# Optimization experiments

Hardware: AMD Instinct MI355X
Metric: run time of the kernel (lower is better)

Reference implementation:

```python
import jax, jax.numpy as jnp
import numpy as np

NUM_HEADS = 12

def _elu1(x):
    return jax.nn.elu(x) + 1.0

def setup_inputs() -> dict:
    key = jax.random.key(0)
    ks = jax.random.split(key, 7)
    B, Nq, Nk, D = 8, 4096, 1024, 768
    s = 0.02
    return {
        "x_query": jax.random.normal(ks[0], (B, Nq, D), dtype=jnp.float32),
        "x_key_value": jax.random.normal(ks[1], (B, Nk, D), dtype=jnp.float32),
        "Wq": jax.random.normal(ks[2], (D, D), dtype=jnp.float32) * s,
        "Wk": jax.random.normal(ks[3], (D, D), dtype=jnp.float32) * s,
        "Wv": jax.random.normal(ks[4], (D, D), dtype=jnp.float32) * s,
        "Wo": jax.random.normal(ks[5], (D, D), dtype=jnp.float32) * s,
        "bo": jax.random.normal(ks[6], (D,), dtype=jnp.float32) * s,
    }

def reference(x_query, x_key_value, Wq, Wk, Wv, Wo, bo):
    B, Nq, D = x_query.shape
    Nk = x_key_value.shape[1]
    H = NUM_HEADS
    hd = D // H
    # projections (torch Linear: x @ W.T), split heads -> [B, H, N, hd]
    q = (x_query @ Wq.T).reshape(B, Nq, H, hd).transpose(0, 2, 1, 3)
    k = (x_key_value @ Wk.T).reshape(B, Nk, H, hd).transpose(0, 2, 1, 3)
    v = (x_key_value @ Wv.T).reshape(B, Nk, H, hd).transpose(0, 2, 1, 3)
    q = _elu1(q)
    k = _elu1(k)
    # kv: [B,H,hd,hd]; k_sum: [B,H,hd]
    kv = jnp.einsum('bhnd,bhne->bhde', k, v)
    k_sum = k.sum(axis=2)
    z = 1.0 / (jnp.einsum('bhqd,bhd->bhq', q, k_sum) + 1e-6)  # [B,H,Nq]
    attn_out = jnp.einsum('bhqd,bhde->bhqe', q, kv) * z[..., None]
    attn_out = attn_out.transpose(0, 2, 1, 3).reshape(B, Nq, D)
    return attn_out @ Wo.T + bo
```

## Files before the change

kernel.cpp:

```cpp
#include <hip/hip_runtime.h>

typedef _Float16 half8_t __attribute__((ext_vector_type(8)));
typedef _Float16 half4_t __attribute__((ext_vector_type(4)));
typedef float    float4_t __attribute__((ext_vector_type(4)));

#define DIM 768

#define GLOAD16(g, l) __builtin_amdgcn_global_load_lds(                        \
    (const __attribute__((address_space(1))) void*)(g),                        \
    (__attribute__((address_space(3))) void*)(l), 16, 0, 0)

#define MFMA16(a, b, c) __builtin_amdgcn_mfma_f32_16x16x32_f16((a), (b), (c), 0, 0, 0)

__global__ __launch_bounds__(256) void cast_all(
    const float* __restrict__ xq,  const float* __restrict__ xkv,
    const float* __restrict__ Wq,  const float* __restrict__ Wk,
    const float* __restrict__ Wv,  const float* __restrict__ Wo,
    _Float16* __restrict__ dq, _Float16* __restrict__ dkv,
    _Float16* __restrict__ dW )
{
    int i = blockIdx.x * 256 + threadIdx.x;
    const float* s; _Float16* d; int off;
    if (i < 3145728)      { s = xq;  d = dq;  off = i; }
    else if (i < 3932160) { s = xkv; d = dkv; off = i - 3145728; }
    else {
        int j = i - 3932160;
        int w = j / 73728;  off = j - w * 73728;
        s = (w == 0) ? Wq : (w == 1) ? Wk : (w == 2) ? Wv : Wo;
        d = dW + (size_t)w * 589824;
    }
    float4_t f0 = *(const float4_t*)&s[(size_t)off * 8];
    float4_t f1 = *(const float4_t*)&s[(size_t)off * 8 + 4];
    half8_t h;
    #pragma unroll
    for (int e = 0; e < 4; ++e) { h[e] = (_Float16)f0[e]; h[e + 4] = (_Float16)f1[e]; }
    *(half8_t*)&d[(size_t)off * 8] = h;
}

__device__ __forceinline__ void gemm_core(const _Float16* __restrict__ A,
                                          const _Float16* __restrict__ W,
                                          int row0, int col0,
                                          _Float16* lds, float4_t acc[8][2])
{
    const int tid  = threadIdx.x;
    const int wid  = tid >> 6, lane = tid & 63;
    const int wr   = wid >> 2;
    const int wc   = wid & 3;
    const int lr   = lane & 15;
    const int lkg  = lane >> 4;
    const int x    = lr & 7;

    const int  srow = wid * 8 + (lane >> 3);
    const int  sg   = ((lane & 7) ^ (lane >> 3)) * 8;
    const _Float16* Ast = A + (size_t)(row0 + srow) * DIM + sg;
    const _Float16* Bst = W + (size_t)(col0 + srow) * DIM + sg;

#define LDSA(s) (&lds[(s) * 24576])
#define LDSB(s) (&lds[(s) * 24576 + 16384])
#define STAGE_A(t, s, j) GLOAD16(Ast + (size_t)(t) * 64 + (size_t)(j) * 64 * DIM, \
                                 LDSA(s) + (j) * 4096 + wid * 512)
#define STAGE_B(t, s, j) GLOAD16(Bst + (size_t)(t) * 64 + (size_t)(j) * 64 * DIM, \
                                 LDSB(s) + (j) * 4096 + wid * 512)

    const int ard = (wr * 128 + lr) * 64;
    const int brd = (wc * 32 + lr) * 64;
    const int g0  = (lkg ^ x) * 8;
    const int g1  = g0 ^ 32;

    STAGE_A(0, 0, 0); STAGE_A(0, 0, 1); STAGE_A(0, 0, 2); STAGE_A(0, 0, 3);
    STAGE_B(0, 0, 0); STAGE_B(0, 0, 1);
    STAGE_A(1, 1, 0); STAGE_A(1, 1, 1); STAGE_A(1, 1, 2); STAGE_A(1, 1, 3);
    STAGE_B(1, 1, 0); STAGE_B(1, 1, 1);
    asm volatile("s_waitcnt vmcnt(6)" ::: "memory");
    __builtin_amdgcn_s_barrier();

    int s = 0, s2 = 2;
    for (int t = 0; t < 12; ++t) {
        const _Float16* Asl = LDSA(s);
        const _Float16* Bsl = LDSB(s);
        const bool pf = (t < 10);

        half8_t bf[2][2];
        bf[0][0] = *(const half8_t*)&Bsl[brd + g0];
        bf[0][1] = *(const half8_t*)&Bsl[brd + g1];
        bf[1][0] = *(const half8_t*)&Bsl[brd + 1024 + g0];
        bf[1][1] = *(const half8_t*)&Bsl[brd + 1024 + g1];
        half8_t af0[4][2];
        #pragma unroll
        for (int i = 0; i < 4; ++i) {
            af0[i][0] = *(const half8_t*)&Asl[ard + i * 1024 + g0];
            af0[i][1] = *(const half8_t*)&Asl[ard + i * 1024 + g1];
        }
        if (pf) { STAGE_A(t + 2, s2, 0); STAGE_A(t + 2, s2, 1); STAGE_A(t + 2, s2, 2); }
        __builtin_amdgcn_s_barrier();
        asm volatile("s_waitcnt lgkmcnt(0)" ::: "memory");
        __builtin_amdgcn_sched_barrier(0);
        __builtin_amdgcn_s_setprio(1);
        #pragma unroll
        for (int i = 0; i < 4; ++i)
            #pragma unroll
            for (int ni = 0; ni < 2; ++ni) {
                acc[i][ni] = MFMA16(af0[i][0], bf[ni][0], acc[i][ni]);
                acc[i][ni] = MFMA16(af0[i][1], bf[ni][1], acc[i][ni]);
            }
        __builtin_amdgcn_s_setprio(0);
        __builtin_amdgcn_sched_barrier(0);
        __builtin_amdgcn_s_barrier();

        half8_t af1[4][2];
        #pragma unroll
        for (int i = 0; i < 4; ++i) {
            af1[i][0] = *(const half8_t*)&Asl[ard + 4096 + i * 1024 + g0];
            af1[i][1] = *(const half8_t*)&Asl[ard + 4096 + i * 1024 + g1];
        }
        if (pf) { STAGE_A(t + 2, s2, 3); STAGE_B(t + 2, s2, 0); STAGE_B(t + 2, s2, 1); }
        __builtin_amdgcn_s_barrier();
        asm volatile("s_waitcnt lgkmcnt(0)" ::: "memory");
        __builtin_amdgcn_sched_barrier(0);
        __builtin_amdgcn_s_setprio(1);
        #pragma unroll
        for (int i = 0; i < 4; ++i)
            #pragma unroll
            for (int ni = 0; ni < 2; ++ni) {
                acc[4 + i][ni] = MFMA16(af1[i][0], bf[ni][0], acc[4 + i][ni]);
                acc[4 + i][ni] = MFMA16(af1[i][1], bf[ni][1], acc[4 + i][ni]);
            }
        __builtin_amdgcn_s_setprio(0);
        __builtin_amdgcn_sched_barrier(0);

        if (t < 11) {
            if (pf) asm volatile("s_waitcnt vmcnt(6)" ::: "memory");
            else    asm volatile("s_waitcnt vmcnt(0)" ::: "memory");
            __builtin_amdgcn_s_barrier();
        }
        s  = (s  == 2) ? 0 : s  + 1;
        s2 = (s2 == 2) ? 0 : s2 + 1;
    }
#undef LDSA
#undef LDSB
#undef STAGE_A
#undef STAGE_B
}

__global__ __launch_bounds__(512) void proj_qkv(
    const _Float16* __restrict__ xq16, const _Float16* __restrict__ xkv16,
    const _Float16* __restrict__ Wq16, const _Float16* __restrict__ Wk16,
    const _Float16* __restrict__ Wv16,
    _Float16* __restrict__ q16, _Float16* __restrict__ k16,
    _Float16* __restrict__ v16)
{
    __shared__ __align__(16) _Float16 lds[3 * 24576];

    const int cpx = gridDim.x >> 3;
    int bid = (blockIdx.x & 7) * cpx + (blockIdx.x >> 3);

    const _Float16 *A, *W; _Float16* O; bool elu;
    int brow, bcol;
    if (bid < 768) {
        A = xq16; W = Wq16; O = q16; elu = true;
        brow = bid / 6; bcol = bid - brow * 6;
    } else {
        int u = bid - 768;
        int mat = u / 192;  u -= mat * 192;
        A = xkv16; W = mat ? Wv16 : Wk16; O = mat ? v16 : k16; elu = !mat;
        brow = u / 6; bcol = u - brow * 6;
    }
    const int row0 = brow * 256, col0 = bcol * 128;

    float4_t acc[8][2] = {};
    gemm_core(A, W, row0, col0, lds, acc);

    const int wid = threadIdx.x >> 6, lane = threadIdx.x & 63;
    const int wr = wid >> 2, wc = wid & 3, lr = lane & 15, lkg = lane >> 4;
    #pragma unroll
    for (int mi = 0; mi < 8; ++mi) {
        #pragma unroll
        for (int ni = 0; ni < 2; ++ni) {
            #pragma unroll
            for (int e = 0; e < 4; ++e) {
                int r = row0 + wr * 128 + mi * 16 + lkg * 4 + e;
                int c = col0 + wc * 32 + ni * 16 + lr;
                float v = acc[mi][ni][e];
                if (elu) v = (v > 0.0f) ? (v + 1.0f) : __expf(v);
                O[(size_t)r * DIM + c] = (_Float16)v;
            }
        }
    }
}

__global__ __launch_bounds__(512) void out_proj(
    const _Float16* __restrict__ a16, const _Float16* __restrict__ Wo16,
    const float* __restrict__ bo, float* __restrict__ out)
{
    __shared__ __align__(16) _Float16 lds[3 * 24576];

    const int cpx = gridDim.x >> 3;
    int bid = (blockIdx.x & 7) * cpx + (blockIdx.x >> 3);
    const int brow = bid / 6, bcol = bid - brow * 6;
    const int row0 = brow * 256, col0 = bcol * 128;

    float4_t acc[8][2] = {};
    gemm_core(a16, Wo16, row0, col0, lds, acc);

    const int wid = threadIdx.x >> 6, lane = threadIdx.x & 63;
    const int wr = wid >> 2, wc = wid & 3, lr = lane & 15, lkg = lane >> 4;
    #pragma unroll
    for (int mi = 0; mi < 8; ++mi) {
        #pragma unroll
        for (int ni = 0; ni < 2; ++ni) {
            #pragma unroll
            for (int e = 0; e < 4; ++e) {
                int r = row0 + wr * 128 + mi * 16 + lkg * 4 + e;
                int c = col0 + wc * 32 + ni * 16 + lr;
                out[(size_t)r * DIM + c] = acc[mi][ni][e] + bo[c];
            }
        }
    }
}

__global__ __launch_bounds__(256) void kv_reduce(const _Float16* __restrict__ k16,
                                                 const _Float16* __restrict__ v16,
                                                 float* __restrict__ kvh,
                                                 float* __restrict__ ksum)
{
    __shared__ __align__(16) _Float16 K[128][64];
    __shared__ __align__(16) _Float16 V[128][64];
    const int chunk = blockIdx.x;
    const int bh    = blockIdx.y;
    const int b = bh / 12, h = bh % 12;
    const int tid = threadIdx.x;

    const size_t base = ((size_t)b * 1024 + (size_t)chunk * 128) * DIM + h * 64;
    #pragma unroll
    for (int j = 0; j < 4; ++j) {
        int idx = j * 256 + tid;
        int r = idx >> 3, c = (idx & 7) * 8;
        *(half8_t*)&K[r][c] = *(const half8_t*)&k16[base + (size_t)r * DIM + c];
        *(half8_t*)&V[r][c] = *(const half8_t*)&v16[base + (size_t)r * DIM + c];
    }
    __syncthreads();

    const int d0 = (tid & 15) * 4;
    const int e0 = (tid >> 4) * 4;
    float acc[4][4] = {};
    #pragma unroll 4
    for (int n = 0; n < 128; ++n) {
        half4_t kd = *(const half4_t*)&K[n][d0];
        half4_t ve = *(const half4_t*)&V[n][e0];
        #pragma unroll
        for (int i = 0; i < 4; ++i)
            #pragma unroll
            for (int j = 0; j < 4; ++j)
                acc[i][j] += (float)ve[i] * (float)kd[j];
    }
    float* kvp = kvh + (size_t)bh * 64 * 64;
    #pragma unroll
    for (int i = 0; i < 4; ++i)
        #pragma unroll
        for (int j = 0; j < 4; ++j)
            atomicAdd(&kvp[(e0 + i) * 64 + d0 + j], acc[i][j]);

    if (tid < 64) {
        float s = 0.0f;
        for (int n = 0; n < 128; ++n) s += (float)K[n][tid];
        atomicAdd(&ksum[bh * 64 + tid], s);
    }
}

__global__ __launch_bounds__(256) void attn_kernel(_Float16* __restrict__ q16,
                                                   const float* __restrict__ kvh,
                                                   const float* __restrict__ ksum)
{
    __shared__ __align__(16) _Float16 Q[128][72];
    __shared__ __align__(16) _Float16 Bv[64][72];
    __shared__ float S[64];
    __shared__ float Z[128];

    const int h    = blockIdx.x;
    const int rb   = blockIdx.y;
    const int row0 = rb * 128;
    const int b    = row0 >> 12;
    const int bh   = b * 12 + h;
    const int tid  = threadIdx.x;

    #pragma unroll
    for (int j = 0; j < 4; ++j) {
        int idx = j * 256 + tid;
        int r = idx >> 3, c = (idx & 7) * 8;
        *(half8_t*)&Q[r][c] =
            *(const half8_t*)&q16[(size_t)(row0 + r) * DIM + h * 64 + c];
    }
    #pragma unroll
    for (int j = 0; j < 4; ++j) {
        int idx = j * 256 + tid;
        int r = idx >> 4, c = (idx & 15) * 4;
        float4_t f = *(const float4_t*)&kvh[((size_t)bh * 64 + r) * 64 + c];
        half4_t hh;
        #pragma unroll
        for (int e = 0; e < 4; ++e) hh[e] = (_Float16)f[e];
        *(half4_t*)&Bv[r][c] = hh;
    }
    if (tid < 64) S[tid] = ksum[bh * 64 + tid];
    __syncthreads();

    if (tid < 128) {
        float dot = 0.0f;
        #pragma unroll 8
        for (int d = 0; d < 64; ++d) dot += (float)Q[tid][d] * S[d];
        Z[tid] = 1.0f / (dot + 1e-6f);
    }
    __syncthreads();

    const int w = tid >> 6, lane = tid & 63;
    const int lr = lane & 15, lkg = lane >> 4;
    float4_t acc[2][4] = {};
    #pragma unroll
    for (int kc = 0; kc < 2; ++kc) {
        half8_t aF[2], bF[4];
        #pragma unroll
        for (int mi = 0; mi < 2; ++mi)
            aF[mi] = *(const half8_t*)&Q[w * 32 + mi * 16 + lr][kc * 32 + lkg * 8];
        #pragma unroll
        for (int ni = 0; ni < 4; ++ni)
            bF[ni] = *(const half8_t*)&Bv[ni * 16 + lr][kc * 32 + lkg * 8];
        #pragma unroll
        for (int mi = 0; mi < 2; ++mi)
            #pragma unroll
            for (int ni = 0; ni < 4; ++ni)
                acc[mi][ni] = MFMA16(aF[mi], bF[ni], acc[mi][ni]);
    }
    #pragma unroll
    for (int mi = 0; mi < 2; ++mi) {
        #pragma unroll
        for (int ni = 0; ni < 4; ++ni) {
            #pragma unroll
            for (int e = 0; e < 4; ++e) {
                int r = w * 32 + mi * 16 + lkg * 4 + e;
                float v = acc[mi][ni][e] * Z[r];
                q16[(size_t)(row0 + r) * DIM + h * 64 + ni * 16 + lr] = (_Float16)v;
            }
        }
    }
}

extern "C" void kernel_launch(void* const* d_in, const int* in_sizes, int n_in,
                              void* d_out, int out_size, void* d_ws, size_t ws_size,
                              hipStream_t stream)
{
    const float* xq  = (const float*)d_in[0];
    const float* xkv = (const float*)d_in[1];
    const float* Wq  = (const float*)d_in[2];
    const float* Wk  = (const float*)d_in[3];
    const float* Wv  = (const float*)d_in[4];
    const float* Wo  = (const float*)d_in[5];
    const float* bo  = (const float*)d_in[6];

    char* ws = (char*)d_ws;
    const size_t SZ_Q16   = (size_t)32768 * 768 * 2;
    const size_t SZ_XKV16 = (size_t)8192 * 768 * 2;
    const size_t SZ_W16   = (size_t)768 * 768 * 2;
    const size_t SZ_KVH   = (size_t)96 * 64 * 64 * 4;
    const size_t SZ_KSUM  = (size_t)96 * 64 * 4;

    _Float16* q16   = (_Float16*)(ws);
    _Float16* xkv16 = (_Float16*)(ws + SZ_Q16);
    _Float16* Wq16  = (_Float16*)(ws + SZ_Q16 + SZ_XKV16);
    _Float16* Wk16  = (_Float16*)(ws + SZ_Q16 + SZ_XKV16 + SZ_W16);
    _Float16* Wv16  = (_Float16*)(ws + SZ_Q16 + SZ_XKV16 + 2 * SZ_W16);
    _Float16* Wo16  = (_Float16*)(ws + SZ_Q16 + SZ_XKV16 + 3 * SZ_W16);
    float*    kvh   = (float*)   (ws + SZ_Q16 + SZ_XKV16 + 4 * SZ_W16);
    float*    ksum  = (float*)   (ws + SZ_Q16 + SZ_XKV16 + 4 * SZ_W16 + SZ_KVH);

    char* ob = (char*)d_out;
    _Float16* xq16 = (_Float16*)(ob);
    _Float16* k16  = (_Float16*)(ob + 50331648);
    _Float16* v16  = (_Float16*)(ob + 50331648 + 12582912);
    float*    out  = (float*)d_out;

    cast_all<<<16512, 256, 0, stream>>>(xq, xkv, Wq, Wk, Wv, Wo,
                                        xq16, xkv16, Wq16);
    hipMemsetAsync(kvh, 0, SZ_KVH + SZ_KSUM, stream);

    proj_qkv<<<1152, 512, 0, stream>>>(xq16, xkv16, Wq16, Wk16, Wv16,
                                       q16, k16, v16);

    kv_reduce<<<dim3(8, 96), 256, 0, stream>>>(k16, v16, kvh, ksum);
    attn_kernel<<<dim3(12, 256), 256, 0, stream>>>(q16, kvh, ksum);

    out_proj<<<768, 512, 0, stream>>>(q16, Wo16, bo, out);
}
```

Before: 224.4 us.

## Use smaller 128x128 tile GEMM with 4 waves for QKV projection

The QKV projection GEMM moves from a 256x128 tile with 8 waves and a 64-wide K step to a new 128x128 tile with 4 waves, a 32-wide K step and a 3-stage LDS ring of 16 KB per stage. It launches twice as many blocks and allows up to 3 blocks per CU, aiming for higher occupancy and better latency hiding. The old core is renamed and kept only for the output projection. The tradeoff is lower arithmetic intensity per tile, more global traffic per FLOP, and an unswizzled LDS layout that may cause bank conflicts.

```diff
diff --git a/kernel.cpp b/kernel.cpp
--- a/kernel.cpp
+++ b/kernel.cpp
@@ -37,10 +37,124 @@
     *(half8_t*)&d[(size_t)off * 8] = h;
 }
 
-__device__ __forceinline__ void gemm_core(const _Float16* __restrict__ A,
-                                          const _Float16* __restrict__ W,
-                                          int row0, int col0,
-                                          _Float16* lds, float4_t acc[8][2])
+__device__ __forceinline__ void gemm_hi(const _Float16* __restrict__ A,
+                                        const _Float16* __restrict__ W,
+                                        int row0, int col0,
+                                        _Float16* lds, float4_t acc[4][4])
+{
+    const int tid  = threadIdx.x;
+    const int wid  = tid >> 6, lane = tid & 63;
+    const int wr   = wid >> 1, wc = wid & 1;
+
+    const int srow = 2 * wid * 16 + (lane & 15);
+    const int sk   = (lane >> 4) * 8;
+    const _Float16* As0 = A + (size_t)(row0 + srow) * DIM + sk;
+    const _Float16* As1 = As0 + (size_t)16 * DIM;
+    const _Float16* Bs0 = W + (size_t)(col0 + srow) * DIM + sk;
+    const _Float16* Bs1 = Bs0 + (size_t)16 * DIM;
+
+#define STAGE(t, s) do {                                                       \
+        GLOAD16(As0 + (t) * 32, &lds[(s) * 8192 + (2*wid    ) * 512]);         \
+        GLOAD16(As1 + (t) * 32, &lds[(s) * 8192 + (2*wid + 1) * 512]);         \
+        GLOAD16(Bs0 + (t) * 32, &lds[(s) * 8192 + 4096 + (2*wid    ) * 512]);  \
+        GLOAD16(Bs1 + (t) * 32, &lds[(s) * 8192 + 4096 + (2*wid + 1) * 512]);  \
+    } while (0)
+
+    const int ab = (4 * wr) * 512 + lane * 8;
+    const int bb = 4096 + (4 * wc) * 512 + lane * 8;
+
+    STAGE(0, 0);
+    STAGE(1, 1);
+    asm volatile("s_waitcnt vmcnt(4)" ::: "memory");
+    __builtin_amdgcn_s_barrier();
+    __builtin_amdgcn_sched_barrier(0);
+
+    int s = 0, s2 = 2;
+    for (int t = 0; t < 24; ++t) {
+        const _Float16* sl = &lds[s * 8192];
+
+        half8_t af[4], bf[4];
+        #pragma unroll
+        for (int mi = 0; mi < 4; ++mi)
+            af[mi] = *(const half8_t*)&sl[ab + mi * 512];
+        #pragma unroll
+        for (int ni = 0; ni < 4; ++ni)
+            bf[ni] = *(const half8_t*)&sl[bb + ni * 512];
+        if (t < 22) STAGE(t + 2, s2);
+
+        asm volatile("s_waitcnt lgkmcnt(0)" ::: "memory");
+        __builtin_amdgcn_sched_barrier(0);
+        __builtin_amdgcn_s_setprio(1);
+        #pragma unroll
+        for (int mi = 0; mi < 4; ++mi)
+            #pragma unroll
+            for (int ni = 0; ni < 4; ++ni)
+                acc[mi][ni] = MFMA16(af[mi], bf[ni], acc[mi][ni]);
+        __builtin_amdgcn_s_setprio(0);
+        __builtin_amdgcn_sched_barrier(0);
+
+        if (t < 23) {
+            if (t < 22) asm volatile("s_waitcnt vmcnt(4)" ::: "memory");
+            else        asm volatile("s_waitcnt vmcnt(0)" ::: "memory");
+            __builtin_amdgcn_s_barrier();
+            __builtin_amdgcn_sched_barrier(0);
+        }
+        s  = (s  == 2) ? 0 : s  + 1;
+        s2 = (s2 == 2) ? 0 : s2 + 1;
+    }
+#undef STAGE
+}
+
+__global__ __launch_bounds__(256, 3) void proj_qkv(
+    const _Float16* __restrict__ xq16, const _Float16* __restrict__ xkv16,
+    const _Float16* __restrict__ Wq16, const _Float16* __restrict__ Wk16,
+    const _Float16* __restrict__ Wv16,
+    _Float16* __restrict__ q16, _Float16* __restrict__ k16,
+    _Float16* __restrict__ v16)
+{
+    __shared__ __align__(16) _Float16 lds[3 * 8192];
+
+    const int cpx = gridDim.x >> 3;
+    int bid = (blockIdx.x & 7) * cpx + (blockIdx.x >> 3);
+
+    const _Float16 *A, *W; _Float16* O; bool elu;
+    int brow, bcol;
+    if (bid < 1536) {
+        A = xq16; W = Wq16; O = q16; elu = true;
+        brow = bid / 6; bcol = bid - brow * 6;
+    } else {
+        int u = bid - 1536;
+        int mat = u / 384;  u -= mat * 384;
+        A = xkv16; W = mat ? Wv16 : Wk16; O = mat ? v16 : k16; elu = !mat;
+        brow = u / 6; bcol = u - brow * 6;
+    }
+    const int row0 = brow * 128, col0 = bcol * 128;
+
+    float4_t acc[4][4] = {};
+    gemm_hi(A, W, row0, col0, lds, acc);
+
+    const int wid = threadIdx.x >> 6, lane = threadIdx.x & 63;
+    const int wr = wid >> 1, wc = wid & 1, lr = lane & 15, lkg = lane >> 4;
+    #pragma unroll
+    for (int mi = 0; mi < 4; ++mi) {
+        #pragma unroll
+        for (int ni = 0; ni < 4; ++ni) {
+            #pragma unroll
+            for (int e = 0; e < 4; ++e) {
+                int r = row0 + wr * 64 + mi * 16 + lkg * 4 + e;
+                int c = col0 + wc * 64 + ni * 16 + lr;
+                float v = acc[mi][ni][e];
+                if (elu) v = (v > 0.0f) ? (v + 1.0f) : __expf(v);
+                O[(size_t)r * DIM + c] = (_Float16)v;
+            }
+        }
+    }
+}
+
+__device__ __forceinline__ void gemm_r4(const _Float16* __restrict__ A,
+                                        const _Float16* __restrict__ W,
+                                        int row0, int col0,
+                                        _Float16* lds, float4_t acc[8][2])
 {
     const int tid  = threadIdx.x;
     const int wid  = tid >> 6, lane = tid & 63;
@@ -142,52 +256,6 @@
 #undef STAGE_B
 }
 
-__global__ __launch_bounds__(512) void proj_qkv(
-    const _Float16* __restrict__ xq16, const _Float16* __restrict__ xkv16,
-    const _Float16* __restrict__ Wq16, const _Float16* __restrict__ Wk16,
-    const _Float16* __restrict__ Wv16,
-    _Float16* __restrict__ q16, _Float16* __restrict__ k16,
-    _Float16* __restrict__ v16)
-{
-    __shared__ __align__(16) _Float16 lds[3 * 24576];
-
-    const int cpx = gridDim.x >> 3;
-    int bid = (blockIdx.x & 7) * cpx + (blockIdx.x >> 3);
-
-    const _Float16 *A, *W; _Float16* O; bool elu;
-    int brow, bcol;
-    if (bid < 768) {
-        A = xq16; W = Wq16; O = q16; elu = true;
-        brow = bid / 6; bcol = bid - brow * 6;
-    } else {
-        int u = bid - 768;
-        int mat = u / 192;  u -= mat * 192;
-        A = xkv16; W = mat ? Wv16 : Wk16; O = mat ? v16 : k16; elu = !mat;
-        brow = u / 6; bcol = u - brow * 6;
-    }
-    const int row0 = brow * 256, col0 = bcol * 128;
-
-    float4_t acc[8][2] = {};
-    gemm_core(A, W, row0, col0, lds, acc);
-
-    const int wid = threadIdx.x >> 6, lane = threadIdx.x & 63;
-    const int wr = wid >> 2, wc = wid & 3, lr = lane & 15, lkg = lane >> 4;
-    #pragma unroll
-    for (int mi = 0; mi < 8; ++mi) {
-        #pragma unroll
-        for (int ni = 0; ni < 2; ++ni) {
-            #pragma unroll
-            for (int e = 0; e < 4; ++e) {
-                int r = row0 + wr * 128 + mi * 16 + lkg * 4 + e;
-                int c = col0 + wc * 32 + ni * 16 + lr;
-                float v = acc[mi][ni][e];
-                if (elu) v = (v > 0.0f) ? (v + 1.0f) : __expf(v);
-                O[(size_t)r * DIM + c] = (_Float16)v;
-            }
-        }
-    }
-}
-
 __global__ __launch_bounds__(512) void out_proj(
     const _Float16* __restrict__ a16, const _Float16* __restrict__ Wo16,
     const float* __restrict__ bo, float* __restrict__ out)
@@ -200,7 +268,7 @@
     const int row0 = brow * 256, col0 = bcol * 128;
 
     float4_t acc[8][2] = {};
-    gemm_core(a16, Wo16, row0, col0, lds, acc);
+    gemm_r4(a16, Wo16, row0, col0, lds, acc);
 
     const int wid = threadIdx.x >> 6, lane = threadIdx.x & 63;
     const int wr = wid >> 2, wc = wid & 3, lr = lane & 15, lkg = lane >> 4;
@@ -381,7 +449,7 @@
                                         xq16, xkv16, Wq16);
     hipMemsetAsync(kvh, 0, SZ_KVH + SZ_KSUM, stream);
 
-    proj_qkv<<<1152, 512, 0, stream>>>(xq16, xkv16, Wq16, Wk16, Wv16,
+    proj_qkv<<<2304, 256, 0, stream>>>(xq16, xkv16, Wq16, Wk16, Wv16,
                                        q16, k16, v16);
 
     kv_reduce<<<dim3(8, 96), 256, 0, stream>>>(k16, v16, kvh, ksum);
```

Measured after the change: 255.5 us. 1.14x slower.
